# Kernel optimization log

Measured on AMD Instinct MI355X. Metric: run time of the kernel, lower is better.

The kernel has to match this reference:

```python
import jax, jax.numpy as jnp
import numpy as np

D = 2  # spatial dimension


def _conv_contract(image, filt, in_k, out_k):
    """Tensor convolution + contraction on a torus.
    image: (in_c, N, N) + (D,)*in_k
    filt:  (out_c, in_c, M, M) + (D,)*in_k + (D,)*out_k
    out:   (out_c, N, N) + (D,)*out_k
    Image tensor indices contract with the first in_k filter tensor indices.
    """
    in_c, N = image.shape[0], image.shape[1]
    out_c, M = filt.shape[0], filt.shape[2]
    di, do = D ** in_k, D ** out_k
    # fold tensor indices into channels: (1, in_c*di, N, N)
    img = jnp.transpose(image.reshape(in_c, N, N, di), (0, 3, 1, 2)).reshape(1, in_c * di, N, N)
    # filter -> (out_c*do, in_c*di, M, M), ordering (out_c, out_idx, in_c, in_idx)
    f = filt.reshape(out_c, in_c, M, M, di, do)
    f = jnp.transpose(f, (0, 5, 1, 4, 2, 3)).reshape(out_c * do, in_c * di, M, M)
    p = M // 2
    img = jnp.pad(img, ((0, 0), (0, 0), (p, p), (p, p)), mode='wrap')  # torus
    out = jax.lax.conv_general_dilated(
        img, f, window_strides=(1, 1), padding='VALID',
        dimension_numbers=('NCHW', 'OIHW', 'NCHW'))[0]
    out = jnp.transpose(out.reshape(out_c, do, N, N), (0, 2, 3, 1))
    return out.reshape((out_c, N, N) + (D,) * out_k)


def _synth(w, fils):
    # (out_c, in_c, n) x (n, M, M, tensor...) -> (out_c, in_c, M, M, tensor...)
    return jnp.einsum('oik,k...->oi...', w, fils)


def setup_inputs() -> dict:
    key = jax.random.key(0)
    ks = jax.random.split(key, 11)
    r = lambda k, s: jax.random.normal(k, s, dtype=jnp.float32)
    return {
        'x0': r(ks[0], (64, 256, 256)),
        'x1': r(ks[1], (64, 256, 256, 2)),
        'fil0': r(ks[2], (3, 3, 3)),
        'fil1': r(ks[3], (6, 3, 3, 2)),
        'fil2': r(ks[4], (12, 3, 3, 2, 2)),
        'w00': r(ks[5], (64, 64, 3)) * (1.0 / np.sqrt(64 * 3)),
        'w01': r(ks[6], (64, 64, 6)) * (1.0 / np.sqrt(64 * 6)),
        'w10': r(ks[7], (64, 64, 6)) * (1.0 / np.sqrt(64 * 6)),
        'w11': r(ks[8], (64, 64, 12)) * (1.0 / np.sqrt(64 * 12)),
        'b0': r(ks[9], (64, 1, 1)) * 0.05,
        'b1': r(ks[10], (64, 1, 1, 1)) * 0.05,
    }


def reference(x0, x1, fil0, fil1, fil2, w00, w01, w10, w11, b0, b1):
    # accumulate over input blocks for each target (out_k, out_p=0)
    out0 = _conv_contract(x0, _synth(w00, fil0), 0, 0) \
         + _conv_contract(x1, _synth(w10, fil1), 1, 0)
    out1 = _conv_contract(x0, _synth(w01, fil1), 0, 1) \
         + _conv_contract(x1, _synth(w11, fil2), 1, 1)
    # use_bias='auto': plain bias for scalars, mean-scaled bias for tensors
    out0 = out0 + b0
    mean1 = jnp.mean(out1, axis=(1, 2), keepdims=True)  # spatial mean
    out1 = out1 + mean1 * b1
    return (out0, out1)
```

## Files before the change

kernel.cpp:

```cpp
#include <hip/hip_runtime.h>
#include <hip/hip_bf16.h>
#include <string.h>


#define NN 256
#define NPIX 65536
#define OUT1_OFF 4194304
#define XB_CH 4096
#define FG_C 27648
#define FBYT 55296
#define XOFF 55296
#define BUFB 79872

typedef __attribute__((ext_vector_type(8))) short short8;
typedef __attribute__((ext_vector_type(16))) float floatx16;

__device__ __forceinline__ unsigned short f2b(float x) {
    unsigned int u; memcpy(&u, &x, 4);
    return (unsigned short)((u + 0x7FFFu + ((u >> 16) & 1u)) >> 16);
}
__device__ __forceinline__ float b2f16(unsigned short u) {
    unsigned int v = ((unsigned int)u) << 16; float f; memcpy(&f, &v, 4); return f;
}
__device__ __forceinline__ unsigned int pack2(float a, float b) {
    return (unsigned int)f2b(a) | ((unsigned int)f2b(b) << 16);
}

__global__ __launch_bounds__(256) void prep_kernel(const float* __restrict__ x0,
                                                   const float* __restrict__ x1,
                                                   unsigned short* __restrict__ Xb,
                                                   float* __restrict__ partial) {
    const int t = threadIdx.x;
    const int w = t >> 6, tx = t & 63;
    const int bxs = blockIdx.x;
    const int yg = ((bxs & 7) << 3) | (bxs >> 3);
    const int y = yg * 4 + w;
    const int c = blockIdx.y;
    const int col0 = tx * 4;

    unsigned int u[4][8];
    float sum[16];
    if (c < 4) {
        #pragma unroll
        for (int j = 0; j < 8; j++) {
            const float4 a = *(const float4*)(x0 + (size_t)(16 * c + 2 * j) * NPIX + y * NN + col0);
            const float4 b = *(const float4*)(x0 + (size_t)(16 * c + 2 * j + 1) * NPIX + y * NN + col0);
            u[0][j] = pack2(a.x, b.x);
            u[1][j] = pack2(a.y, b.y);
            u[2][j] = pack2(a.z, b.z);
            u[3][j] = pack2(a.w, b.w);
            sum[2 * j]     = a.x + a.y + a.z + a.w;
            sum[2 * j + 1] = b.x + b.y + b.z + b.w;
        }
    } else {
        #pragma unroll
        for (int j = 0; j < 8; j++) {
            int i = 8 * (c - 4) + j;
            const float* base = x1 + ((size_t)(i * 256 + y) * 256 + col0) * 2;
            const float4 p0 = *(const float4*)(base);
            const float4 p1 = *(const float4*)(base + 4);
            u[0][j] = pack2(p0.x, p0.y);
            u[1][j] = pack2(p0.z, p0.w);
            u[2][j] = pack2(p1.x, p1.y);
            u[3][j] = pack2(p1.z, p1.w);
            sum[2 * j]     = p0.x + p0.z + p1.x + p1.z;
            sum[2 * j + 1] = p0.y + p0.w + p1.y + p1.w;
        }
    }
    char* rowp = (char*)(Xb + ((size_t)y * 12 + c) * XB_CH);
    #pragma unroll
    for (int cc = 0; cc < 4; cc++) {
        int col = col0 + cc;
        int sw = (col & 7) << 4;
        *(uint4*)(rowp + ((col * 32)      ^ sw)) = make_uint4(u[cc][0], u[cc][1], u[cc][2], u[cc][3]);
        *(uint4*)(rowp + ((col * 32 + 16) ^ sw)) = make_uint4(u[cc][4], u[cc][5], u[cc][6], u[cc][7]);
    }
    #pragma unroll
    for (int cl = 0; cl < 16; cl++)
        #pragma unroll
        for (int d = 1; d < 64; d <<= 1) sum[cl] += __shfl_xor(sum[cl], d, 64);
    if (tx < 16) partial[(c * 16 + tx) * 256 + y] = sum[tx];
}

__global__ void synth_kernel(const float* __restrict__ fil0, const float* __restrict__ fil1,
                             const float* __restrict__ fil2,
                             const float* __restrict__ w00, const float* __restrict__ w01,
                             const float* __restrict__ w10, const float* __restrict__ w11,
                             unsigned short* __restrict__ Fg) {
    int idx = blockIdx.x * 256 + threadIdx.x;
    if (idx >= 12 * 192 * 144) return;
    int kpos = idx % 144;
    int co   = (idx / 144) % 192;
    int c    = idx / (144 * 192);
    int tap = kpos >> 4, cl = kpos & 15;
    float s = 0.0f;
    {
        int cin = c * 16 + cl;
        if (co < 64) {
            if (cin < 64) {
                for (int k = 0; k < 3; k++)
                    s += w00[(co * 64 + cin) * 3 + k] * fil0[k * 9 + tap];
            } else {
                int i = (cin - 64) >> 1, t = (cin - 64) & 1;
                for (int k = 0; k < 6; k++)
                    s += w10[(co * 64 + i) * 6 + k] * fil1[(k * 9 + tap) * 2 + t];
            }
        } else {
            int o = (co - 64) >> 1, u = (co - 64) & 1;
            if (cin < 64) {
                for (int k = 0; k < 6; k++)
                    s += w01[(o * 64 + cin) * 6 + k] * fil1[(k * 9 + tap) * 2 + u];
            } else {
                int i = (cin - 64) >> 1, t = (cin - 64) & 1;
                for (int k = 0; k < 12; k++)
                    s += w11[(o * 64 + i) * 12 + k] * fil2[((k * 9 + tap) * 2 + t) * 2 + u];
            }
        }
    }
    int swz = (tap < 8) ? ((co & 7) << 3) : (((co >> 2) & 1) << 3);
    int off = ((tap * 16 + (cl & 8)) ^ swz) + (cl & 7);
    Fg[((size_t)c * 192 + co) * 144 + off] = f2b(s);
}

__global__ void meanbx_kernel(const unsigned short* __restrict__ Fg,
                              const float* __restrict__ partial,
                              const float* __restrict__ b1, float* __restrict__ meanb) {
    __shared__ float mX[192];
    __shared__ float rd[4];
    const int c1 = blockIdx.x;
    const int t = threadIdx.x;
    if (t < 192) {
        const float4* p = (const float4*)(partial + (size_t)t * 256);
        float s = 0.0f;
        for (int j = 0; j < 64; j++) { float4 v = p[j]; s += v.x + v.y + v.z + v.w; }
        mX[t] = s * (1.0f / 65536.0f);
    }
    __syncthreads();
    float s = 0.0f;
    for (int e = t; e < 1728; e += 256) {
        int c = e / 144, r = e - c * 144;
        int tap = r >> 4, cl = r & 15;
        int swz = (tap < 8) ? ((c1 & 7) << 3) : (((c1 >> 2) & 1) << 3);
        int off = ((tap * 16 + (cl & 8)) ^ swz) + (cl & 7);
        s += b2f16(Fg[((size_t)c * 192 + 64 + c1) * 144 + off]) * mX[c * 16 + cl];
    }
#pragma unroll
    for (int d = 1; d < 64; d <<= 1) s += __shfl_xor(s, d, 64);
    if ((t & 63) == 0) rd[t >> 6] = s;
    __syncthreads();
    if (t == 0) meanb[c1] = (rd[0] + rd[1] + rd[2] + rd[3]) * b1[c1 >> 1];
}

__global__ __launch_bounds__(512, 2) void conv_kernel(
    const unsigned short* __restrict__ Xb, const unsigned short* __restrict__ Fg,
    const float* __restrict__ b0, const float* __restrict__ meanb,
    float* __restrict__ out) {

    __shared__ __align__(16) char lds[2 * BUFB];

    const int tid = threadIdx.x;
    const int bx = blockIdx.x;
    const int y = ((bx & 7) << 5) | (bx >> 3);
    const int l = tid & 63, w = tid >> 6;
    const int wm = w >> 2, wn = w & 3;
    const int nw = wn * 64;
    const int l31 = l & 31;
    const int hi16 = (l >> 5) << 4;
    const int swzA = (l & 7) << 4;
    const int swzA8 = (l & 4) << 2;

    int rowterm[3];
#pragma unroll
    for (int f = 0; f < 3; f++)
        rowterm[f] = (wm * 96 + f * 32 + l31) * 288;

    int addrB[9][2];
#pragma unroll
    for (int t = 0; t < 9; t++) {
        int r = t / 3, dx = t % 3 - 1;
#pragma unroll
        for (int g = 0; g < 2; g++) {
            int colw = (nw + g * 32 + l31 + dx) & 255;
            addrB[t][g] = XOFF + r * 8192 + ((colw * 32 + hi16) ^ ((colw & 7) << 4));
        }
    }

    floatx16 acc[3][2];
#pragma unroll
    for (int f = 0; f < 3; f++)
#pragma unroll
        for (int g = 0; g < 2; g++)
#pragma unroll
            for (int r = 0; r < 16; r++) acc[f][g][r] = 0.f;

    auto stage = [&](int c, int bsel) {
        char* base = lds + bsel * BUFB;
        for (int s = w; s < 78; s += 8) {
            const unsigned short* g;
            char* lb;
            if (s < 54) {
                g = Fg + (size_t)c * FG_C + s * 512;
                lb = base + s * 1024;
            } else {
                int j = s - 54;
                int r = j >> 3, p = j & 7;
                int yr = (y + r + 255) & 255;
                g = Xb + ((size_t)yr * 12 + c) * XB_CH + p * 512;
                lb = base + XOFF + r * 8192 + p * 1024;
            }
            __builtin_amdgcn_global_load_lds(
                (const __attribute__((address_space(1))) unsigned int*)(g + l * 8),
                (__attribute__((address_space(3))) unsigned int*)lb, 16, 0, 0);
        }
    };

    stage(0, 0);
    __syncthreads();

    int cur = 0;
    for (int c = 0; c < 12; c++) {
        if (c < 11) stage(c + 1, cur ^ 1);
        const char* fb = lds + cur * BUFB;
#pragma unroll
        for (int t = 0; t < 9; t++) {
            short8 A[3], B[2];
            int kterm = (t < 8) ? ((t * 32 + hi16) ^ swzA)
                                : ((256 + hi16) ^ swzA8);
#pragma unroll
            for (int f = 0; f < 3; f++)
                A[f] = *(const short8*)(fb + rowterm[f] + kterm);
#pragma unroll
            for (int g = 0; g < 2; g++)
                B[g] = *(const short8*)(fb + addrB[t][g]);
#pragma unroll
            for (int f = 0; f < 3; f++)
#pragma unroll
                for (int g = 0; g < 2; g++)
                    acc[f][g] = __builtin_amdgcn_mfma_f32_32x32x16_bf16(A[f], B[g], acc[f][g], 0, 0, 0);
        }
        __syncthreads();
        cur ^= 1;
    }

    const int hi4 = (l >> 5) * 4;
#pragma unroll
    for (int f = 0; f < 3; f++) {
#pragma unroll
        for (int g = 0; g < 2; g++) {
            int col = nw + g * 32 + l31;
#pragma unroll
            for (int rr = 0; rr < 4; rr++) {
                int co0 = wm * 96 + f * 32 + hi4 + 8 * rr;
                if (co0 < 64) {
#pragma unroll
                    for (int q = 0; q < 4; q++)
                        out[(size_t)(co0 + q) * NPIX + y * NN + col] =
                            acc[f][g][rr * 4 + q] + b0[co0 + q];
                } else {
#pragma unroll
                    for (int q = 0; q < 4; q += 2) {
                        int c1 = co0 + q - 64;
                        float2 v = make_float2(acc[f][g][rr * 4 + q] + meanb[c1],
                                               acc[f][g][rr * 4 + q + 1] + meanb[c1 + 1]);
                        *((float2*)(out + OUT1_OFF) + ((size_t)(c1 >> 1) * NPIX + y * NN + col)) = v;
                    }
                }
            }
        }
    }
}

extern "C" void kernel_launch(void* const* d_in, const int* in_sizes, int n_in,
                              void* d_out, int out_size, void* d_ws, size_t ws_size,
                              hipStream_t stream) {
    const float* x0   = (const float*)d_in[0];
    const float* x1   = (const float*)d_in[1];
    const float* fil0 = (const float*)d_in[2];
    const float* fil1 = (const float*)d_in[3];
    const float* fil2 = (const float*)d_in[4];
    const float* w00  = (const float*)d_in[5];
    const float* w01  = (const float*)d_in[6];
    const float* w10  = (const float*)d_in[7];
    const float* w11  = (const float*)d_in[8];
    const float* b0   = (const float*)d_in[9];
    const float* b1   = (const float*)d_in[10];

    unsigned short* Xb = (unsigned short*)d_ws;
    unsigned short* Fg = (unsigned short*)((char*)d_ws + 25165824);
    float* partial     = (float*)((char*)d_ws + 25829376);
    float* meanb       = (float*)((char*)d_ws + 26025984);
    float* out = (float*)d_out;

    prep_kernel<<<dim3(64, 12), 256, 0, stream>>>(x0, x1, Xb, partial);

    synth_kernel<<<(12 * 192 * 144 + 255) / 256, 256, 0, stream>>>(
        fil0, fil1, fil2, w00, w01, w10, w11, Fg);

    meanbx_kernel<<<128, 256, 0, stream>>>(Fg, partial, b1, meanb);

    conv_kernel<<<dim3(256), 512, 0, stream>>>(Xb, Fg, b0, meanb, out);
}
```

Baseline: 174.3 us.

## Split conv output channels across grid y and drop double buffering

The conv kernel now launches a 256x3 grid of 256-thread blocks, each covering 64 output channels instead of all 192. LDS becomes a single 43 KB buffer with no prefetch, so more blocks can be resident to hide load latency. The spatial-mean reduction is also moved out of meanbx into a separate parallel meanx kernel, shortening that serial step. In exchange the input tile is loaded three times from global memory, there is an extra kernel launch, and the loss of explicit load/compute overlap now has to be covered by occupancy.

```diff
diff --git a/kernel.cpp b/kernel.cpp
--- a/kernel.cpp
+++ b/kernel.cpp
@@ -7,10 +7,9 @@
 #define NPIX 65536
 #define OUT1_OFF 4194304
 #define XB_CH 4096
-#define FG_C 27648
-#define FBYT 55296
-#define XOFF 55296
-#define BUFB 79872
+#define FTILE 18432
+#define XOFF2 18432
+#define CBUF 43008
 
 typedef __attribute__((ext_vector_type(8))) short short8;
 typedef __attribute__((ext_vector_type(16))) float floatx16;
@@ -122,19 +121,24 @@
     Fg[((size_t)c * 192 + co) * 144 + off] = f2b(s);
 }
 
+__global__ void meanx_kernel(const float* __restrict__ partial, float* __restrict__ mXg) {
+    const int cc = blockIdx.x;
+    const int l = threadIdx.x;
+    float4 v = ((const float4*)(partial + (size_t)cc * 256))[l];
+    float s = v.x + v.y + v.z + v.w;
+#pragma unroll
+    for (int d = 1; d < 64; d <<= 1) s += __shfl_xor(s, d, 64);
+    if (l == 0) mXg[cc] = s * (1.0f / 65536.0f);
+}
+
 __global__ void meanbx_kernel(const unsigned short* __restrict__ Fg,
-                              const float* __restrict__ partial,
+                              const float* __restrict__ mXg,
                               const float* __restrict__ b1, float* __restrict__ meanb) {
     __shared__ float mX[192];
     __shared__ float rd[4];
     const int c1 = blockIdx.x;
     const int t = threadIdx.x;
-    if (t < 192) {
-        const float4* p = (const float4*)(partial + (size_t)t * 256);
-        float s = 0.0f;
-        for (int j = 0; j < 64; j++) { float4 v = p[j]; s += v.x + v.y + v.z + v.w; }
-        mX[t] = s * (1.0f / 65536.0f);
-    }
+    if (t < 192) mX[t] = mXg[t];
     __syncthreads();
     float s = 0.0f;
     for (int e = t; e < 1728; e += 256) {
@@ -151,28 +155,28 @@
     if (t == 0) meanb[c1] = (rd[0] + rd[1] + rd[2] + rd[3]) * b1[c1 >> 1];
 }
 
-__global__ __launch_bounds__(512, 2) void conv_kernel(
+__global__ __launch_bounds__(256, 3) void conv_kernel(
     const unsigned short* __restrict__ Xb, const unsigned short* __restrict__ Fg,
     const float* __restrict__ b0, const float* __restrict__ meanb,
     float* __restrict__ out) {
 
-    __shared__ __align__(16) char lds[2 * BUFB];
+    __shared__ __align__(16) char lds[CBUF];
 
     const int tid = threadIdx.x;
     const int bx = blockIdx.x;
     const int y = ((bx & 7) << 5) | (bx >> 3);
+    const int m0 = blockIdx.y * 64;
     const int l = tid & 63, w = tid >> 6;
-    const int wm = w >> 2, wn = w & 3;
-    const int nw = wn * 64;
+    const int nw = w * 64;
     const int l31 = l & 31;
     const int hi16 = (l >> 5) << 4;
     const int swzA = (l & 7) << 4;
     const int swzA8 = (l & 4) << 2;
 
-    int rowterm[3];
-#pragma unroll
-    for (int f = 0; f < 3; f++)
-        rowterm[f] = (wm * 96 + f * 32 + l31) * 288;
+    int rowterm[2];
+#pragma unroll
+    for (int f = 0; f < 2; f++)
+        rowterm[f] = (f * 32 + l31) * 288;
 
     int addrB[9][2];
 #pragma unroll
@@ -181,76 +185,67 @@
 #pragma unroll
         for (int g = 0; g < 2; g++) {
             int colw = (nw + g * 32 + l31 + dx) & 255;
-            addrB[t][g] = XOFF + r * 8192 + ((colw * 32 + hi16) ^ ((colw & 7) << 4));
-        }
-    }
-
-    floatx16 acc[3][2];
-#pragma unroll
-    for (int f = 0; f < 3; f++)
+            addrB[t][g] = XOFF2 + r * 8192 + ((colw * 32 + hi16) ^ ((colw & 7) << 4));
+        }
+    }
+
+    floatx16 acc[2][2];
+#pragma unroll
+    for (int f = 0; f < 2; f++)
 #pragma unroll
         for (int g = 0; g < 2; g++)
 #pragma unroll
             for (int r = 0; r < 16; r++) acc[f][g][r] = 0.f;
 
-    auto stage = [&](int c, int bsel) {
-        char* base = lds + bsel * BUFB;
-        for (int s = w; s < 78; s += 8) {
+    for (int c = 0; c < 12; c++) {
+        for (int s = w; s < 42; s += 4) {
             const unsigned short* g;
             char* lb;
-            if (s < 54) {
-                g = Fg + (size_t)c * FG_C + s * 512;
-                lb = base + s * 1024;
+            if (s < 18) {
+                g = Fg + ((size_t)c * 192 + m0) * 144 + s * 512;
+                lb = lds + s * 1024;
             } else {
-                int j = s - 54;
+                int j = s - 18;
                 int r = j >> 3, p = j & 7;
                 int yr = (y + r + 255) & 255;
                 g = Xb + ((size_t)yr * 12 + c) * XB_CH + p * 512;
-                lb = base + XOFF + r * 8192 + p * 1024;
+                lb = lds + XOFF2 + r * 8192 + p * 1024;
             }
             __builtin_amdgcn_global_load_lds(
                 (const __attribute__((address_space(1))) unsigned int*)(g + l * 8),
                 (__attribute__((address_space(3))) unsigned int*)lb, 16, 0, 0);
         }
-    };
-
-    stage(0, 0);
-    __syncthreads();
-
-    int cur = 0;
-    for (int c = 0; c < 12; c++) {
-        if (c < 11) stage(c + 1, cur ^ 1);
-        const char* fb = lds + cur * BUFB;
+        __syncthreads();
+
 #pragma unroll
         for (int t = 0; t < 9; t++) {
-            short8 A[3], B[2];
+            short8 A[2], B[2];
             int kterm = (t < 8) ? ((t * 32 + hi16) ^ swzA)
                                 : ((256 + hi16) ^ swzA8);
 #pragma unroll
-            for (int f = 0; f < 3; f++)
-                A[f] = *(const short8*)(fb + rowterm[f] + kterm);
+            for (int f = 0; f < 2; f++)
+                A[f] = *(const short8*)(lds + rowterm[f] + kterm);
 #pragma unroll
             for (int g = 0; g < 2; g++)
-                B[g] = *(const short8*)(fb + addrB[t][g]);
-#pragma unroll
-            for (int f = 0; f < 3; f++)
+                B[g] = *(const short8*)(lds + addrB[t][g]);
+#pragma unroll
+            for (int f = 0; f < 2; f++)
 #pragma unroll
                 for (int g = 0; g < 2; g++)
                     acc[f][g] = __builtin_amdgcn_mfma_f32_32x32x16_bf16(A[f], B[g], acc[f][g], 0, 0, 0);
         }
         __syncthreads();
-        cur ^= 1;
     }
 
     const int hi4 = (l >> 5) * 4;
 #pragma unroll
-    for (int f = 0; f < 3; f++) {
+    for (int f = 0; f < 2; f++) {
 #pragma unroll
         for (int g = 0; g < 2; g++) {
             int col = nw + g * 32 + l31;
 #pragma unroll
             for (int rr = 0; rr < 4; rr++) {
-                int co0 = wm * 96 + f * 32 + hi4 + 8 * rr;
+                int co0 = m0 + f * 32 + hi4 + 8 * rr;
                 if (co0 < 64) {
 #pragma unroll
                     for (int q = 0; q < 4; q++)
@@ -289,6 +284,7 @@
     unsigned short* Fg = (unsigned short*)((char*)d_ws + 25165824);
     float* partial     = (float*)((char*)d_ws + 25829376);
     float* meanb       = (float*)((char*)d_ws + 26025984);
+    float* mXg         = (float*)((char*)d_ws + 26026496);
     float* out = (float*)d_out;
 
     prep_kernel<<<dim3(64, 12), 256, 0, stream>>>(x0, x1, Xb, partial);
@@ -296,7 +292,9 @@
     synth_kernel<<<(12 * 192 * 144 + 255) / 256, 256, 0, stream>>>(
         fil0, fil1, fil2, w00, w01, w10, w11, Fg);
 
-    meanbx_kernel<<<128, 256, 0, stream>>>(Fg, partial, b1, meanb);
-
-    conv_kernel<<<dim3(256), 512, 0, stream>>>(Xb, Fg, b0, meanb, out);
-}
+    meanx_kernel<<<192, 64, 0, stream>>>(partial, mXg);
+
+    meanbx_kernel<<<128, 256, 0, stream>>>(Fg, mXg, b1, meanb);
+
+    conv_kernel<<<dim3(256, 3), 256, 0, stream>>>(Xb, Fg, b0, meanb, out);
+}
```

After: 173.8 us. About the same (-0.2%).
